# Performance work log

Hardware: AMD Instinct MI355X
Metric: run time of the kernel (lower is better)

## Reference

```python
import jax, jax.numpy as jnp
import numpy as np

HID = 5120       # hidden_size
H = 32           # num_heads (TP shard)
Q_RANK = 1536    # q_lora_rank
KV_RANK = 512    # kv_lora_rank
D_NOPE = 128     # qk_nope_head_dim
D_ROPE = 64      # qk_rope_head_dim
DV = 128         # v_head_dim
Q_HEAD = D_NOPE + D_ROPE
T = 2048
EPS = 1e-6
ROPE_BASE = 10000.0
SCALE = Q_HEAD ** -0.5
NEG = jnp.finfo(jnp.float32).min


def rmsnorm(x, w):
    return x * jax.lax.rsqrt(jnp.mean(x * x, axis=-1, keepdims=True) + EPS) * w


def rope(x, pos):
    # half-split (GPT-NeoX style) rotary; the torch module permutes weights in
    # _update_pe so that interleaved RoPE becomes exactly this half-split form.
    half = x.shape[-1] // 2
    inv = 1.0 / (ROPE_BASE ** (jnp.arange(half, dtype=jnp.float32) / half))
    ang = pos.astype(jnp.float32)[:, None] * inv          # [T, half]
    cos, sin = jnp.cos(ang), jnp.sin(ang)
    if x.ndim == 3:                                       # [T, H, D]
        cos, sin = cos[:, None, :], sin[:, None, :]
    x1, x2 = jnp.split(x, 2, axis=-1)
    return jnp.concatenate([x1 * cos - x2 * sin, x2 * cos + x1 * sin], axis=-1)


def setup_inputs() -> dict:
    key = jax.random.key(0)
    ks = jax.random.split(key, 10)
    s = 0.02
    return {
        'hidden_states': jax.random.normal(ks[0], (1, T, HID), jnp.float32),
        'position_ids': jnp.arange(T, dtype=jnp.int64),
        'w_q_a': jax.random.normal(ks[1], (Q_RANK, HID), jnp.float32) * s,
        'q_a_ln_w': jnp.ones((Q_RANK,), jnp.float32),
        'w_q_b': jax.random.normal(ks[2], (H * Q_HEAD, Q_RANK), jnp.float32) * s,
        'w_kv_a': jax.random.normal(ks[3], (KV_RANK + D_ROPE, HID), jnp.float32) * s,
        'kv_a_ln_w': jnp.ones((KV_RANK,), jnp.float32),
        'w_kc': jax.random.normal(ks[4], (H, D_NOPE, KV_RANK), jnp.float32) * s,
        'w_vc': jax.random.normal(ks[5], (H, KV_RANK, DV), jnp.float32) * s,
        'w_o': jax.random.normal(ks[6], (HID, H * DV), jnp.float32) * s,
    }


def reference(hidden_states, position_ids, w_q_a, q_a_ln_w, w_q_b, w_kv_a,
              kv_a_ln_w, w_kc, w_vc, w_o):
    h = hidden_states[0]                                   # [T, HID]
    t = h.shape[0]
    # q low-rank path: q_a_proj -> rmsnorm -> q_b_proj
    q = rmsnorm(h @ w_q_a.T, q_a_ln_w) @ w_q_b.T           # [T, H*Q_HEAD]
    q = q.reshape(t, H, Q_HEAD)
    q_nope, q_pe = q[..., :D_NOPE], q[..., D_NOPE:]
    # absorb kv_b (w_kc): project q into the latent kv space
    q_lat = jnp.einsum('thn,hnk->thk', q_nope, w_kc)       # [T, H, KV_RANK]
    # kv low-rank path (MQA-style shared latent)
    ckv_full = h @ w_kv_a.T                                # [T, KV_RANK+D_ROPE]
    ckv = rmsnorm(ckv_full[:, :KV_RANK], kv_a_ln_w)        # [T, KV_RANK]
    k_pe = rope(ckv_full[:, KV_RANK:], position_ids)       # [T, D_ROPE]
    q_pe = rope(q_pe, position_ids)                        # [T, H, D_ROPE]
    # full query/key in latent+pe space; key/value shared across heads
    qf = jnp.concatenate([q_lat, q_pe], axis=-1)           # [T, H, KV_RANK+D_ROPE]
    kf = jnp.concatenate([ckv, k_pe], axis=-1)             # [T, KV_RANK+D_ROPE]
    scores = jnp.einsum('thd,sd->hts', qf, kf) * SCALE     # [H, T, T]
    causal = jnp.tril(jnp.ones((t, t), dtype=bool))
    scores = jnp.where(causal[None], scores, NEG)
    p = jax.nn.softmax(scores, axis=-1)
    o = jnp.einsum('hts,sk->thk', p, ckv)                  # [T, H, KV_RANK]
    o = jnp.einsum('thk,hkv->thv', o, w_vc)                # [T, H, DV]
    out = o.reshape(t, H * DV) @ w_o.T                     # [T, HID]
    return out[None]
```

## Files before the change

### kernel.cpp

```cpp
#include <hip/hip_runtime.h>
#include <hip/hip_bf16.h>
#include <type_traits>

typedef __attribute__((ext_vector_type(8))) short short8;
typedef __attribute__((ext_vector_type(4))) float f32x4;
using bf16 = __hip_bfloat16;

#define T_SEQ 2048
#define NH 32
#define SCALE_F 0.07216878364870323f

__device__ inline unsigned short f2bf(float f) {
    unsigned u = __builtin_bit_cast(unsigned, f);
    return (unsigned short)((u + 0x7fffu + ((u >> 16) & 1u)) >> 16);
}

__device__ inline void gload_lds16(const void* g, void* l) {
    __builtin_amdgcn_global_load_lds(
        (const __attribute__((address_space(1))) unsigned*)g,
        (__attribute__((address_space(3))) unsigned*)l, 16, 0, 0);
}

template <typename TC>
__global__ __launch_bounds__(512, 2) void gemm8p_kernel(
    const bf16* __restrict__ A, const bf16* __restrict__ B, TC* __restrict__ C,
    int K, int lda, int ldb, int ldc)
{
    extern __shared__ char Lds[];
    const int nwg = gridDim.x * gridDim.y;
    const int lin = blockIdx.y * gridDim.x + blockIdx.x;
    const int lin2 = (lin & 7) * (nwg >> 3) + (lin >> 3);
    const int bm = (lin2 / gridDim.x) * 256, bn = (lin2 % gridDim.x) * 256;
    const int tid = threadIdx.x, lane = tid & 63, w = tid >> 6;
    const int l15 = lane & 15, lg = lane >> 4;
    const int wmr = (w >> 2) * 64;
    const int wnc = (w & 3) * 32;
    const int lrh = lane >> 3;
    const int scolb = ((lane & 7) * 16) ^ ((lane >> 3) << 4);
    const int rdswz = (l15 & 7) << 4;
    const bf16* Ab = A + (long)bm * lda;
    const bf16* Bb = B + (long)bn * ldb;
    const int nt = K >> 6;

    auto stage_half = [&](int tt, int isB, int h) {
        const int buf = tt & 1;
        const int k0 = (tt >= nt ? tt - nt : tt) << 6;
        const bf16* Base = isB ? Bb : Ab;
        const int ld = isB ? ldb : lda;
        const char* g = (const char*)Base
            + ((long)(h * 128 + w * 8 + lrh) * ld + k0) * 2 + scolb;
        char* l = Lds + buf * 65536 + isB * 32768 + h * 16384 + w * 1024;
        gload_lds16(g, l);
        gload_lds16(g + (long)128 * ld, l + 8192);
    };

    f32x4 acc[4][4][2] = {};
    stage_half(0, 0, 0); stage_half(0, 1, 1); stage_half(0, 0, 1);
    stage_half(0, 1, 0); stage_half(1, 0, 0); stage_half(1, 1, 1);
    asm volatile("s_waitcnt vmcnt(4)" ::: "memory");
    __builtin_amdgcn_s_barrier();

    for (int t = 0; t < nt; ++t) {
        const char* Bufp = Lds + (t & 1) * 65536;
        short8 aF[4][2], bF[2][2];
        #define ARD(mh, fi, ks) \
            (*(const short8*)(Bufp + (mh) * 16384 + (wmr + (fi) * 16 + l15) * 128 \
                              + (((ks) * 64 + lg * 16) ^ rdswz)))
        #define BRD(nh, nj, ks) \
            (*(const short8*)(Bufp + 32768 + (nh) * 16384 + (wnc + (nj) * 16 + l15) * 128 \
                              + (((ks) * 64 + lg * 16) ^ rdswz)))
        #define MFMA16(q) \
            __builtin_amdgcn_s_setprio(1); \
            _Pragma("unroll") for (int ks = 0; ks < 2; ++ks) \
            _Pragma("unroll") for (int fi = 0; fi < 4; ++fi) \
            _Pragma("unroll") for (int nj = 0; nj < 2; ++nj) \
                acc[q][fi][nj] = __builtin_amdgcn_mfma_f32_16x16x32_bf16( \
                    aF[fi][ks], bF[nj][ks], acc[q][fi][nj], 0, 0, 0); \
            __builtin_amdgcn_s_setprio(0);

        #pragma unroll
        for (int fi = 0; fi < 4; ++fi) { aF[fi][0] = ARD(0, fi, 0); aF[fi][1] = ARD(0, fi, 1); }
        #pragma unroll
        for (int nj = 0; nj < 2; ++nj) { bF[nj][0] = BRD(0, nj, 0); bF[nj][1] = BRD(0, nj, 1); }
        stage_half(t + 1, 0, 1);
        asm volatile("s_waitcnt lgkmcnt(8)" ::: "memory");
        __builtin_amdgcn_s_barrier();
        asm volatile("s_waitcnt lgkmcnt(0)" ::: "memory");
        __builtin_amdgcn_sched_barrier(0);
        MFMA16(0)
        __builtin_amdgcn_s_barrier();
        #pragma unroll
        for (int nj = 0; nj < 2; ++nj) { bF[nj][0] = BRD(1, nj, 0); bF[nj][1] = BRD(1, nj, 1); }
        stage_half(t + 1, 1, 0);
        __builtin_amdgcn_s_barrier();
        asm volatile("s_waitcnt lgkmcnt(0)" ::: "memory");
        __builtin_amdgcn_sched_barrier(0);
        MFMA16(1)
        __builtin_amdgcn_s_barrier();
        #pragma unroll
        for (int fi = 0; fi < 4; ++fi) { aF[fi][0] = ARD(1, fi, 0); aF[fi][1] = ARD(1, fi, 1); }
        stage_half(t + 2, 0, 0);
        __builtin_amdgcn_s_barrier();
        asm volatile("s_waitcnt lgkmcnt(0)" ::: "memory");
        __builtin_amdgcn_sched_barrier(0);
        MFMA16(2)
        __builtin_amdgcn_s_barrier();
        #pragma unroll
        for (int nj = 0; nj < 2; ++nj) { bF[nj][0] = BRD(0, nj, 0); bF[nj][1] = BRD(0, nj, 1); }
        stage_half(t + 2, 1, 1);
        __builtin_amdgcn_s_barrier();
        asm volatile("s_waitcnt lgkmcnt(0)" ::: "memory");
        __builtin_amdgcn_sched_barrier(0);
        MFMA16(3)
        asm volatile("s_waitcnt vmcnt(4)" ::: "memory");
        __builtin_amdgcn_s_barrier();
        #undef ARD
        #undef BRD
        #undef MFMA16
    }
    asm volatile("s_waitcnt vmcnt(0)" ::: "memory");
    const int QMH[4] = {0, 0, 1, 1}, QNH[4] = {0, 1, 1, 0};
    #pragma unroll
    for (int q = 0; q < 4; ++q)
        #pragma unroll
        for (int fi = 0; fi < 4; ++fi)
            #pragma unroll
            for (int nj = 0; nj < 2; ++nj)
                #pragma unroll
                for (int i = 0; i < 4; ++i) {
                    const int row = bm + QMH[q] * 128 + wmr + fi * 16 + lg * 4 + i;
                    const int col = bn + QNH[q] * 128 + wnc + nj * 16 + l15;
                    if constexpr (std::is_same<TC, float>::value)
                        C[(long)row * ldc + col] = acc[q][fi][nj][i];
                    else
                        ((unsigned short*)C)[(long)row * ldc + col] = f2bf(acc[q][fi][nj][i]);
                }
}

template <typename TC>
__global__ __launch_bounds__(256, 2) void gemmhw_kernel(
    const bf16* __restrict__ A, const bf16* __restrict__ B, TC* __restrict__ C,
    int K, int lda, int ldb, int ldc,
    long aStride, long bStride, long cStride)
{
    const int z = blockIdx.z;
    A += (long)z * aStride; B += (long)z * bStride; C += (long)z * cStride;
    const int bm = blockIdx.y * 256, bn = blockIdx.x * 128;
    __shared__ __align__(16) short As[2][256 * 32];
    __shared__ __align__(16) short Bs[2][128 * 32];
    const int tid = threadIdx.x, lane = tid & 63, w = tid >> 6;
    const int l15 = lane & 15, lg = lane >> 4;
    const int wm = w >> 1, wn = w & 1;
    const int sx = (lane & 7) ^ (lane >> 3);
    const int lrh = lane >> 3;
    const int srp = sx >> 2;
    const int scol = (sx & 3) * 8;
    const bf16* Ab = A + (long)bm * lda;
    const bf16* Bb = B + (long)bn * ldb;

    auto stage = [&](int buf, int k0) {
        #pragma unroll
        for (int jj = 0; jj < 4; ++jj) {
            const int j = w * 4 + jj;
            const int srow = 2 * (j * 8 + lrh) + srp;
            gload_lds16(Ab + (long)srow * lda + k0 + scol, &As[buf][j * 512]);
        }
        #pragma unroll
        for (int jj = 0; jj < 2; ++jj) {
            const int j = w * 2 + jj;
            const int srow = 2 * (j * 8 + lrh) + srp;
            gload_lds16(Bb + (long)srow * ldb + k0 + scol, &Bs[buf][j * 512]);
        }
    };

    const int rslot = ((((l15 & 1) << 2) | lg) ^ (l15 >> 1)) << 4;
    const int lrow_lo = l15 >> 1;
    f32x4 acc[8][4] = {};
    const int nt = K >> 5;
    stage(0, 0);
    for (int t = 0; t < nt; ++t) {
        if (t + 1 < nt) {
            stage((t + 1) & 1, (t + 1) << 5);
            asm volatile("s_waitcnt vmcnt(6)" ::: "memory");
        } else {
            asm volatile("s_waitcnt vmcnt(0)" ::: "memory");
        }
        __builtin_amdgcn_s_barrier();
        __builtin_amdgcn_sched_barrier(0);
        const char* Ap = (const char*)&As[t & 1][0];
        const char* Bp = (const char*)&Bs[t & 1][0];
        short8 af[8], bf[4];
        #pragma unroll
        for (int fi = 0; fi < 8; ++fi)
            af[fi] = *(const short8*)(Ap + (wm * 64 + fi * 8 + lrow_lo) * 128 + rslot);
        #pragma unroll
        for (int nj = 0; nj < 4; ++nj)
            bf[nj] = *(const short8*)(Bp + (wn * 32 + nj * 8 + lrow_lo) * 128 + rslot);
        #pragma unroll
        for (int fi = 0; fi < 8; ++fi)
            #pragma unroll
            for (int nj = 0; nj < 4; ++nj)
                acc[fi][nj] = __builtin_amdgcn_mfma_f32_16x16x32_bf16(
                    af[fi], bf[nj], acc[fi][nj], 0, 0, 0);
        asm volatile("s_waitcnt lgkmcnt(0)" ::: "memory");
        __builtin_amdgcn_sched_barrier(0);
        __builtin_amdgcn_s_barrier();
        __builtin_amdgcn_sched_barrier(0);
    }
    #pragma unroll
    for (int fi = 0; fi < 8; ++fi)
        #pragma unroll
        for (int nj = 0; nj < 4; ++nj)
            #pragma unroll
            for (int i = 0; i < 4; ++i) {
                const int row = bm + wm * 128 + fi * 16 + lg * 4 + i;
                const int col = bn + wn * 64 + nj * 16 + l15;
                if constexpr (std::is_same<TC, float>::value)
                    C[(long)row * ldc + col] = acc[fi][nj][i];
                else
                    ((unsigned short*)C)[(long)row * ldc + col] = f2bf(acc[fi][nj][i]);
            }
}

template <typename TC>
__global__ __launch_bounds__(512, 4) void gemm8w_kernel(
    const bf16* __restrict__ A, const bf16* __restrict__ B, TC* __restrict__ C,
    int K, int lda, int ldb, int ldc,
    long aStride, long bStride, long cStride)
{
    const int z = blockIdx.z;
    A += (long)z * aStride; B += (long)z * bStride; C += (long)z * cStride;
    const int nwg = gridDim.x * gridDim.y;
    const int lin = blockIdx.y * gridDim.x + blockIdx.x;
    const int lin2 = (lin & 7) * (nwg >> 3) + (lin >> 3);
    const int bm = (lin2 / gridDim.x) * 128, bn = (lin2 % gridDim.x) * 128;
    __shared__ __align__(16) short As[2][128 * 64];
    __shared__ __align__(16) short Bs[2][128 * 64];
    const int tid = threadIdx.x, lane = tid & 63, w = tid >> 6;
    const int l15 = lane & 15, lg = lane >> 4;
    const int wm = w >> 1, wn = w & 1;
    const int c0 = w * 2, c1 = w * 2 + 1;
    const int srow0 = c0 * 8 + (lane >> 3), srow1 = c1 * 8 + (lane >> 3);
    const int scol = ((lane & 7) * 16) ^ ((lane >> 3) << 4);
    const bf16* Ab = A + (long)bm * lda;
    const bf16* Bb = B + (long)bn * ldb;

    auto stage = [&](int buf, int k0) {
        const char* ag = (const char*)(Ab + k0);
        const char* bg = (const char*)(Bb + k0);
        gload_lds16(ag + (long)srow0 * (lda * 2) + scol, &As[buf][c0 * 512]);
        gload_lds16(ag + (long)srow1 * (lda * 2) + scol, &As[buf][c1 * 512]);
        gload_lds16(bg + (long)srow0 * (ldb * 2) + scol, &Bs[buf][c0 * 512]);
        gload_lds16(bg + (long)srow1 * (ldb * 2) + scol, &Bs[buf][c1 * 512]);
    };

    const int swz = (l15 & 7) << 4;
    f32x4 acc[2][4] = {};
    const int nt = K >> 6;
    stage(0, 0);
    for (int t = 0; t < nt; ++t) {
        if (t + 1 < nt) {
            stage((t + 1) & 1, (t + 1) << 6);
            asm volatile("s_waitcnt vmcnt(4)" ::: "memory");
        } else {
            asm volatile("s_waitcnt vmcnt(0)" ::: "memory");
        }
        __builtin_amdgcn_s_barrier();
        __builtin_amdgcn_sched_barrier(0);
        const char* Ap = (const char*)&As[t & 1][0];
        const char* Bp = (const char*)&Bs[t & 1][0];
        short8 af[2][2], bfv[4][2];
        #pragma unroll
        for (int fi = 0; fi < 2; ++fi)
            #pragma unroll
            for (int ks = 0; ks < 2; ++ks)
                af[fi][ks] = *(const short8*)(Ap + (wm * 32 + fi * 16 + l15) * 128
                                              + ((ks * 64 + lg * 16) ^ swz));
        #pragma unroll
        for (int nj = 0; nj < 4; ++nj)
            #pragma unroll
            for (int ks = 0; ks < 2; ++ks)
                bfv[nj][ks] = *(const short8*)(Bp + (wn * 64 + nj * 16 + l15) * 128
                                               + ((ks * 64 + lg * 16) ^ swz));
        #pragma unroll
        for (int ks = 0; ks < 2; ++ks)
            #pragma unroll
            for (int fi = 0; fi < 2; ++fi)
                #pragma unroll
                for (int nj = 0; nj < 4; ++nj)
                    acc[fi][nj] = __builtin_amdgcn_mfma_f32_16x16x32_bf16(
                        af[fi][ks], bfv[nj][ks], acc[fi][nj], 0, 0, 0);
        asm volatile("s_waitcnt lgkmcnt(0)" ::: "memory");
        __builtin_amdgcn_sched_barrier(0);
        __builtin_amdgcn_s_barrier();
        __builtin_amdgcn_sched_barrier(0);
    }
    #pragma unroll
    for (int fi = 0; fi < 2; ++fi)
        #pragma unroll
        for (int nj = 0; nj < 4; ++nj)
            #pragma unroll
            for (int i = 0; i < 4; ++i) {
                const int row = bm + wm * 32 + fi * 16 + lg * 4 + i;
                const int col = bn + wn * 64 + nj * 16 + l15;
                if constexpr (std::is_same<TC, float>::value)
                    C[(long)row * ldc + col] = acc[fi][nj][i];
                else
                    ((unsigned short*)C)[(long)row * ldc + col] = f2bf(acc[fi][nj][i]);
            }
}

__global__ __launch_bounds__(256) void cvt_kernel(
    const float* __restrict__ in, bf16* __restrict__ out, long n, float scale)
{
    const long i = ((long)blockIdx.x * 256 + threadIdx.x) * 8;
    if (i >= n) return;
    f32x4 a = *(const f32x4*)(in + i), b = *(const f32x4*)(in + i + 4);
    short8 r;
    r[0] = (short)f2bf(a[0] * scale); r[1] = (short)f2bf(a[1] * scale);
    r[2] = (short)f2bf(a[2] * scale); r[3] = (short)f2bf(a[3] * scale);
    r[4] = (short)f2bf(b[0] * scale); r[5] = (short)f2bf(b[1] * scale);
    r[6] = (short)f2bf(b[2] * scale); r[7] = (short)f2bf(b[3] * scale);
    *(short8*)(out + i) = r;
}

__global__ __launch_bounds__(256) void tconv_kernel(
    const float* __restrict__ in, bf16* __restrict__ out)
{
    const int h = blockIdx.z, k0 = blockIdx.x * 32, d0 = blockIdx.y * 32;
    __shared__ float t[32][33];
    const int r = threadIdx.x >> 5, c = threadIdx.x & 31;
    const float* ip = in + ((long)h * 512 + k0) * 128 + d0;
    #pragma unroll
    for (int it = 0; it < 4; ++it)
        t[r + 8 * it][c] = ip[(long)(r + 8 * it) * 128 + c];
    __syncthreads();
    bf16* op = out + ((long)h * 128 + d0) * 512 + k0;
    #pragma unroll
    for (int it = 0; it < 4; ++it)
        op[(long)(r + 8 * it) * 512 + c] = __float2bfloat16(t[c][r + 8 * it]);
}

__global__ __launch_bounds__(256) void rmsnorm_kernel(
    bf16* __restrict__ x, const float* __restrict__ w, int C, int ld)
{
    bf16* row = x + (long)blockIdx.x * ld;
    float ss = 0.f;
    for (int i = threadIdx.x; i < C; i += 256) {
        float v = __bfloat162float(row[i]);
        ss += v * v;
    }
    #pragma unroll
    for (int m = 1; m < 64; m <<= 1) ss += __shfl_xor(ss, m, 64);
    __shared__ float red[4];
    if ((threadIdx.x & 63) == 0) red[threadIdx.x >> 6] = ss;
    __syncthreads();
    ss = red[0] + red[1] + red[2] + red[3];
    float scale = rsqrtf(ss / (float)C + 1e-6f);
    for (int i = threadIdx.x; i < C; i += 256) {
        float v = __bfloat162float(row[i]);
        row[i] = __float2bfloat16(v * scale * w[i]);
    }
}

__global__ __launch_bounds__(256) void ropeq_kernel(bf16* __restrict__ q)
{
    const int t = blockIdx.x;
    #pragma unroll
    for (int it = 0; it < 4; ++it) {
        const int pair = threadIdx.x + 256 * it;
        const int h = pair >> 5, i = pair & 31;
        bf16* base = q + ((long)t * NH + h) * 192;
        float x1 = __bfloat162float(base[128 + i]);
        float x2 = __bfloat162float(base[160 + i]);
        float inv = powf(10000.f, -(float)i / 32.f);
        float ang = (float)t * inv, s, c;
        sincosf(ang, &s, &c);
        base[128 + i] = __float2bfloat16(x1 * c - x2 * s);
        base[160 + i] = __float2bfloat16(x2 * c + x1 * s);
    }
}

__global__ __launch_bounds__(1024) void ropek_kernel(
    const bf16* __restrict__ ckv, bf16* __restrict__ kf, int ld)
{
    const int t = blockIdx.x;
    const int h = threadIdx.x >> 5, i = threadIdx.x & 31;
    float x1 = __bfloat162float(ckv[(long)t * ld + 512 + i]);
    float x2 = __bfloat162float(ckv[(long)t * ld + 544 + i]);
    float inv = powf(10000.f, -(float)i / 32.f);
    float ang = (float)t * inv, s, c;
    sincosf(ang, &s, &c);
    bf16* kb = kf + ((long)h * T_SEQ + t) * 192;
    kb[128 + i] = __float2bfloat16(x1 * c - x2 * s);
    kb[160 + i] = __float2bfloat16(x2 * c + x1 * s);
}

__global__ __launch_bounds__(256, 2) void attn_kernel(
    const bf16* __restrict__ Q,
    const bf16* __restrict__ Kf,
    const bf16* __restrict__ Vt,
    bf16* __restrict__ O,
    const float* __restrict__ WOin, bf16* __restrict__ WOout)
{
    if (blockIdx.x >= 512) {
        const long base = ((long)blockIdx.x - 512) * 16384 + threadIdx.x * 8;
        #pragma unroll
        for (int it = 0; it < 8; ++it) {
            const long i = base + (long)it * 2048;
            f32x4 a = *(const f32x4*)(WOin + i), b = *(const f32x4*)(WOin + i + 4);
            short8 r;
            r[0] = (short)f2bf(a[0]); r[1] = (short)f2bf(a[1]);
            r[2] = (short)f2bf(a[2]); r[3] = (short)f2bf(a[3]);
            r[4] = (short)f2bf(b[0]); r[5] = (short)f2bf(b[1]);
            r[6] = (short)f2bf(b[2]); r[7] = (short)f2bf(b[3]);
            *(short8*)(WOout + i) = r;
        }
        return;
    }
    const int lin = blockIdx.x;
    const int h = (lin & 7) + 8 * ((lin >> 3) & 3);
    const int qraw = lin >> 5;
    const int qblk = (qraw < 8) ? (2 * qraw) : (31 - 2 * qraw);
    const int q0 = qblk * 128;
    const int tid = threadIdx.x, lane = tid & 63, w = tid >> 6;
    const int l15 = lane & 15, lg = lane >> 4;
    const int qw = q0 + w * 32;
    __shared__ __align__(16) short Ks[2][64 * 192];
    __shared__ __align__(16) short Vs[2][128 * 64];

    int ksoff[6];
    #pragma unroll
    for (int j = 0; j < 6; ++j) {
        int o = (w * 6 + j) * 1024 + lane * 16;
        int row = o / 384, col = o % 384;
        ksoff[j] = row * 384 + (col ^ ((row & 7) << 4));
    }
    const int vrow8 = lane >> 3;
    const int vscol = ((lane & 7) * 16) ^ (vrow8 << 4);

    short8 qf[2][6];
    #pragma unroll
    for (int qi = 0; qi < 2; ++qi) {
        const bf16* qp = Q + (long)(qw + qi * 16 + l15) * (NH * 192) + (long)h * 192;
        #pragma unroll
        for (int c = 0; c < 6; ++c) qf[qi][c] = *(const short8*)(qp + c * 32 + lg * 8);
    }

    f32x4 oacc[2][8] = {};
    float mst[2] = {-INFINITY, -INFINITY};
    float lst[2] = {0.f, 0.f};

    const char* kbase0 = (const char*)Kf + (long)h * T_SEQ * 384;
    const char* vbase0 = (const char*)Vt + (long)h * 128 * (T_SEQ * 2);
    const int swz = (l15 & 7) << 4;
    const int nt = (q0 + 128) >> 6;

    auto stage = [&](int t) {
        char* KsB = (char*)&Ks[t & 1][0];
        char* VsB = (char*)&Vs[t & 1][0];
        const char* kb = kbase0 + (long)(t * 64) * 384;
        #pragma unroll
        for (int j = 0; j < 6; ++j)
            gload_lds16(kb + ksoff[j], KsB + (w * 6 + j) * 1024);
        const char* vb = vbase0 + (long)(t * 64) * 2 + vscol;
        #pragma unroll
        for (int j = 0; j < 4; ++j) {
            const int c = w * 4 + j;
            gload_lds16(vb + (long)(c * 8 + vrow8) * (T_SEQ * 2), VsB + c * 1024);
        }
    };

    stage(0);
    for (int t = 0; t < nt; ++t) {
        const int s0 = t * 64;
        if (t + 1 < nt) {
            stage(t + 1);
            asm volatile("s_waitcnt vmcnt(10)" ::: "memory");
        } else {
            asm volatile("s_waitcnt vmcnt(0)" ::: "memory");
        }
        __builtin_amdgcn_s_barrier();
        __builtin_amdgcn_sched_barrier(0);
        if (s0 <= qw + 31) {
            const char* KsB = (const char*)&Ks[t & 1][0];
            const char* VsB = (const char*)&Vs[t & 1][0];
            f32x4 st[2][4] = {};
            __builtin_amdgcn_s_setprio(1);
            #pragma unroll
            for (int cb = 0; cb < 4; ++cb) {
                const int krow = cb * 16 + l15;
                #pragma unroll
                for (int c = 0; c < 6; ++c) {
                    short8 kfr = *(const short8*)(KsB + krow * 384
                                                  + ((c * 64 + lg * 16) ^ swz));
                    st[0][cb] = __builtin_amdgcn_mfma_f32_16x16x32_bf16(kfr, qf[0][c], st[0][cb], 0, 0, 0);
                    st[1][cb] = __builtin_amdgcn_mfma_f32_16x16x32_bf16(kfr, qf[1][c], st[1][cb], 0, 0, 0);
                }
            }
            __builtin_amdgcn_s_setprio(0);
            float pmaxv[2];
            #pragma unroll
            for (int qi = 0; qi < 2; ++qi) {
                const int qg = qw + qi * 16 + l15;
                float pmax = -INFINITY;
                #pragma unroll
                for (int cb = 0; cb < 4; ++cb)
                    #pragma unroll
                    for (int i = 0; i < 4; ++i) {
                        const int kv = s0 + cb * 16 + lg * 4 + i;
                        float v = (kv <= qg) ? st[qi][cb][i] : -INFINITY;
                        st[qi][cb][i] = v;
                        pmax = fmaxf(pmax, v);
                    }
                pmax = fmaxf(pmax, __shfl_xor(pmax, 16, 64));
                pmax = fmaxf(pmax, __shfl_xor(pmax, 32, 64));
                pmaxv[qi] = pmax;
            }
            const bool full = !__all((pmaxv[0] - mst[0] <= 8.f) &&
                                     (pmaxv[1] - mst[1] <= 8.f));
            short8 pb[2][2];
            #pragma unroll
            for (int qi = 0; qi < 2; ++qi) {
                float mm;
                if (full) {
                    const float newm = fmaxf(mst[qi], pmaxv[qi]);
                    mm = (newm == -INFINITY) ? 0.f : newm;
                    const float alpha = __expf(mst[qi] - mm);
                    lst[qi] *= alpha;
                    mst[qi] = newm;
                    #pragma unroll
                    for (int mb = 0; mb < 8; ++mb) oacc[qi][mb] *= alpha;
                } else {
                    mm = mst[qi];
                }
                float ps = 0.f;
                #pragma unroll
                for (int cb = 0; cb < 4; ++cb)
                    #pragma unroll
                    for (int i = 0; i < 4; ++i) {
                        const float e = __expf(st[qi][cb][i] - mm);
                        st[qi][cb][i] = e; ps += e;
                    }
                ps += __shfl_xor(ps, 16, 64);
                ps += __shfl_xor(ps, 32, 64);
                lst[qi] += ps;
                #pragma unroll
                for (int hh = 0; hh < 2; ++hh) {
                    unsigned pk[4];
                    #pragma unroll
                    for (int i = 0; i < 4; ++i)
                        pk[i] = (unsigned)f2bf(st[qi][2 * hh][i])
                              | ((unsigned)f2bf(st[qi][2 * hh + 1][i]) << 16);
                    #pragma unroll
                    for (int j = 0; j < 8; ++j) {
                        const int src = l15 + (((2 * lg + (j >> 2)) & 3) << 4);
                        const unsigned u = (unsigned)__shfl((int)pk[j & 3], src, 64);
                        pb[qi][hh][j] = (short)((lg >> 1) ? (u >> 16) : (u & 0xffffu));
                    }
                }
            }
            __builtin_amdgcn_s_setprio(1);
            #pragma unroll
            for (int mb = 0; mb < 8; ++mb) {
                const int vrow = mb * 16 + l15;
                #pragma unroll
                for (int hh = 0; hh < 2; ++hh) {
                    short8 vfr = *(const short8*)(VsB + vrow * 128
                                                  + ((hh * 64 + lg * 16) ^ swz));
                    oacc[0][mb] = __builtin_amdgcn_mfma_f32_16x16x32_bf16(vfr, pb[0][hh], oacc[0][mb], 0, 0, 0);
                    oacc[1][mb] = __builtin_amdgcn_mfma_f32_16x16x32_bf16(vfr, pb[1][hh], oacc[1][mb], 0, 0, 0);
                }
            }
            __builtin_amdgcn_s_setprio(0);
        }
        __builtin_amdgcn_sched_barrier(0);
        __builtin_amdgcn_s_barrier();
    }
    #pragma unroll
    for (int qi = 0; qi < 2; ++qi) {
        const float inv = 1.f / lst[qi];
        const int qg = qw + qi * 16 + l15;
        #pragma unroll
        for (int mb = 0; mb < 8; ++mb)
            #pragma unroll
            for (int i = 0; i < 4; ++i) {
                const int dv = mb * 16 + lg * 4 + i;
                O[(long)qg * (NH * 128) + h * 128 + dv] = __float2bfloat16(oacc[qi][mb][i] * inv);
            }
    }
}

extern "C" void kernel_launch(void* const* d_in, const int* in_sizes, int n_in,
                              void* d_out, int out_size, void* d_ws, size_t ws_size,
                              hipStream_t stream)
{
    const float* hidden    = (const float*)d_in[0];
    const float* w_q_a     = (const float*)d_in[2];
    const float* q_a_ln_w  = (const float*)d_in[3];
    const float* w_q_b     = (const float*)d_in[4];
    const float* w_kv_a    = (const float*)d_in[5];
    const float* kv_a_ln_w = (const float*)d_in[6];
    const float* w_kc      = (const float*)d_in[7];
    const float* w_vc      = (const float*)d_in[8];
    const float* w_o       = (const float*)d_in[9];
    float* out = (float*)d_out;

    bf16* qckv  = (bf16*)d_ws;
    bf16* qbuf  = qckv  + (long)T_SEQ * 2176;
    bf16* kf    = qbuf  + (long)T_SEQ * 6144;
    bf16* vt    = kf    + (long)NH * T_SEQ * 192;
    bf16* ov    = vt    + (long)NH * 128 * T_SEQ;
    bf16* hb    = ov    + (long)T_SEQ * 4096;
    bf16* wqckv = hb    + (long)T_SEQ * 5120;
    bf16* wqb   = wqckv + (long)2176 * 5120;
    bf16* wkc   = wqb   + (long)6144 * 1536;
    bf16* wvct  = wkc   + (long)NH * 128 * 512;
    bf16* wo    = hb;
    bf16* ckv   = qckv + 1536;

    cvt_kernel<<<dim3(5120), 256, 0, stream>>>(hidden, hb, (long)T_SEQ * 5120, 1.f);
    cvt_kernel<<<dim3(3840), 256, 0, stream>>>(w_q_a, wqckv, (long)1536 * 5120, 1.f);
    cvt_kernel<<<dim3(1440), 256, 0, stream>>>(w_kv_a, wqckv + (long)1536 * 5120,
                                               (long)576 * 5120, 1.f);
    hipMemsetAsync(wqckv + (long)2112 * 5120, 0, (long)64 * 5120 * sizeof(bf16), stream);
    cvt_kernel<<<dim3(4608), 256, 0, stream>>>(w_q_b, wqb, (long)6144 * 1536, SCALE_F);
    cvt_kernel<<<dim3(1024), 256, 0, stream>>>(w_kc, wkc, (long)NH * 128 * 512, 1.f);
    tconv_kernel<<<dim3(16, 4, NH), 256, 0, stream>>>(w_vc, wvct);

    gemm8w_kernel<bf16><<<dim3(17, 16, 1), 512, 0, stream>>>(
        hb, wqckv, qckv, 5120, 5120, 5120, 2176, 0, 0, 0);
    rmsnorm_kernel<<<dim3(T_SEQ), 256, 0, stream>>>(qckv, q_a_ln_w, 1536, 2176);
    rmsnorm_kernel<<<dim3(T_SEQ), 256, 0, stream>>>(ckv, kv_a_ln_w, 512, 2176);
    gemm8p_kernel<bf16><<<dim3(24, 8), 512, 131072, stream>>>(
        qckv, wqb, qbuf, 1536, 2176, 1536, 6144);
    ropeq_kernel<<<dim3(T_SEQ), 256, 0, stream>>>(qbuf);
    ropek_kernel<<<dim3(T_SEQ), 1024, 0, stream>>>(ckv, kf, 2176);
    gemmhw_kernel<bf16><<<dim3(1, 8, NH), 256, 0, stream>>>(
        ckv, wkc, kf, 512, 2176, 512, 192,
        0, (long)128 * 512, (long)T_SEQ * 192);
    gemm8p_kernel<bf16><<<dim3(8, 16), 512, 131072, stream>>>(
        wvct, ckv, vt, 512, 512, 2176, 2048);
    attn_kernel<<<dim3(1792), 256, 0, stream>>>(qbuf, kf, vt, ov, w_o, wo);
    gemm8p_kernel<float><<<dim3(20, 8), 512, 131072, stream>>>(
        ov, wo, out, 4096, 4096, 4096, 5120);
}
```

Measured before the change: 447.0 us.

## Fold weight conversions into first GEMM grid and merge two rmsnorm launches

The w_q_b and w_kc fp32-to-bf16 conversions now run on extra workgroups appended to the q/kv-a GEMM grid, so they overlap with the GEMM instead of running as separate launches beforehand. The two rmsnorm launches are merged into one kernel that picks its row set by block index. The XCD-aware tile remapping in both GEMM kernels is removed in favour of plain blockIdx mapping. This cuts launch count, but the extra conversion blocks compete with GEMM blocks for CUs and bandwidth, and dropping the remap may change L2 locality.

Result: no change. 441.7 us (-1.2%).

```diff
diff --git a/kernel.cpp b/kernel.cpp
--- a/kernel.cpp
+++ b/kernel.cpp
@@ -21,16 +21,23 @@
         (__attribute__((address_space(3))) unsigned*)l, 16, 0, 0);
 }
 
+__device__ inline void cvt8(const float* in, bf16* out, long v, float scale) {
+    f32x4 a = *(const f32x4*)(in + v * 8), b = *(const f32x4*)(in + v * 8 + 4);
+    short8 r;
+    r[0] = (short)f2bf(a[0] * scale); r[1] = (short)f2bf(a[1] * scale);
+    r[2] = (short)f2bf(a[2] * scale); r[3] = (short)f2bf(a[3] * scale);
+    r[4] = (short)f2bf(b[0] * scale); r[5] = (short)f2bf(b[1] * scale);
+    r[6] = (short)f2bf(b[2] * scale); r[7] = (short)f2bf(b[3] * scale);
+    *(short8*)(out + v * 8) = r;
+}
+
 template <typename TC>
 __global__ __launch_bounds__(512, 2) void gemm8p_kernel(
     const bf16* __restrict__ A, const bf16* __restrict__ B, TC* __restrict__ C,
     int K, int lda, int ldb, int ldc)
 {
     extern __shared__ char Lds[];
-    const int nwg = gridDim.x * gridDim.y;
-    const int lin = blockIdx.y * gridDim.x + blockIdx.x;
-    const int lin2 = (lin & 7) * (nwg >> 3) + (lin >> 3);
-    const int bm = (lin2 / gridDim.x) * 256, bn = (lin2 % gridDim.x) * 256;
+    const int bm = blockIdx.y * 256, bn = blockIdx.x * 256;
     const int tid = threadIdx.x, lane = tid & 63, w = tid >> 6;
     const int l15 = lane & 15, lg = lane >> 4;
     const int wmr = (w >> 2) * 64;
@@ -222,21 +229,29 @@
             }
 }
 
+#define GW_NXT 17
+#define GW_EXX 8
 template <typename TC>
 __global__ __launch_bounds__(512, 4) void gemm8w_kernel(
     const bf16* __restrict__ A, const bf16* __restrict__ B, TC* __restrict__ C,
     int K, int lda, int ldb, int ldc,
-    long aStride, long bStride, long cStride)
-{
-    const int z = blockIdx.z;
-    A += (long)z * aStride; B += (long)z * bStride; C += (long)z * cStride;
-    const int nwg = gridDim.x * gridDim.y;
-    const int lin = blockIdx.y * gridDim.x + blockIdx.x;
-    const int lin2 = (lin & 7) * (nwg >> 3) + (lin >> 3);
-    const int bm = (lin2 / gridDim.x) * 128, bn = (lin2 % gridDim.x) * 128;
+    const float* __restrict__ cv1in, bf16* __restrict__ cv1out, long n1v, float s1,
+    const float* __restrict__ cv2in, bf16* __restrict__ cv2out, long n2v)
+{
+    const int tid = threadIdx.x;
+    if (blockIdx.x >= GW_NXT) {
+        const int cb = (blockIdx.x - GW_NXT) * gridDim.y + blockIdx.y;
+        const long stride = (long)GW_EXX * gridDim.y * 512;
+        for (long v = (long)cb * 512 + tid; v < n1v + n2v; v += stride) {
+            if (v < n1v) cvt8(cv1in, cv1out, v, s1);
+            else         cvt8(cv2in, cv2out, v - n1v, 1.f);
+        }
+        return;
+    }
+    const int bm = blockIdx.y * 128, bn = blockIdx.x * 128;
     __shared__ __align__(16) short As[2][128 * 64];
     __shared__ __align__(16) short Bs[2][128 * 64];
-    const int tid = threadIdx.x, lane = tid & 63, w = tid >> 6;
+    const int lane = tid & 63, w = tid >> 6;
     const int l15 = lane & 15, lg = lane >> 4;
     const int wm = w >> 1, wn = w & 1;
     const int c0 = w * 2, c1 = w * 2 + 1;
@@ -313,15 +328,9 @@
 __global__ __launch_bounds__(256) void cvt_kernel(
     const float* __restrict__ in, bf16* __restrict__ out, long n, float scale)
 {
-    const long i = ((long)blockIdx.x * 256 + threadIdx.x) * 8;
-    if (i >= n) return;
-    f32x4 a = *(const f32x4*)(in + i), b = *(const f32x4*)(in + i + 4);
-    short8 r;
-    r[0] = (short)f2bf(a[0] * scale); r[1] = (short)f2bf(a[1] * scale);
-    r[2] = (short)f2bf(a[2] * scale); r[3] = (short)f2bf(a[3] * scale);
-    r[4] = (short)f2bf(b[0] * scale); r[5] = (short)f2bf(b[1] * scale);
-    r[6] = (short)f2bf(b[2] * scale); r[7] = (short)f2bf(b[3] * scale);
-    *(short8*)(out + i) = r;
+    const long i = (long)blockIdx.x * 256 + threadIdx.x;
+    if (i * 8 >= n) return;
+    cvt8(in, out, i, scale);
 }
 
 __global__ __launch_bounds__(256) void tconv_kernel(
@@ -341,10 +350,15 @@
         op[(long)(r + 8 * it) * 512 + c] = __float2bfloat16(t[c][r + 8 * it]);
 }
 
-__global__ __launch_bounds__(256) void rmsnorm_kernel(
-    bf16* __restrict__ x, const float* __restrict__ w, int C, int ld)
-{
-    bf16* row = x + (long)blockIdx.x * ld;
+__global__ __launch_bounds__(256) void rmsnorm2_kernel(
+    bf16* __restrict__ x1, const float* __restrict__ w1, int C1,
+    bf16* __restrict__ x2, const float* __restrict__ w2, int C2, int ld)
+{
+    bf16* row;
+    const float* w;
+    int C;
+    if (blockIdx.x < 2048) { row = x1 + (long)blockIdx.x * ld; w = w1; C = C1; }
+    else { row = x2 + (long)(blockIdx.x - 2048) * ld; w = w2; C = C2; }
     float ss = 0.f;
     for (int i = threadIdx.x; i < C; i += 256) {
         float v = __bfloat162float(row[i]);
@@ -404,18 +418,10 @@
     const float* __restrict__ WOin, bf16* __restrict__ WOout)
 {
     if (blockIdx.x >= 512) {
-        const long base = ((long)blockIdx.x - 512) * 16384 + threadIdx.x * 8;
-        #pragma unroll
-        for (int it = 0; it < 8; ++it) {
-            const long i = base + (long)it * 2048;
-            f32x4 a = *(const f32x4*)(WOin + i), b = *(const f32x4*)(WOin + i + 4);
-            short8 r;
-            r[0] = (short)f2bf(a[0]); r[1] = (short)f2bf(a[1]);
-            r[2] = (short)f2bf(a[2]); r[3] = (short)f2bf(a[3]);
-            r[4] = (short)f2bf(b[0]); r[5] = (short)f2bf(b[1]);
-            r[6] = (short)f2bf(b[2]); r[7] = (short)f2bf(b[3]);
-            *(short8*)(WOout + i) = r;
-        }
+        const long base = ((long)blockIdx.x - 512) * 2048 + threadIdx.x;
+        #pragma unroll
+        for (int it = 0; it < 8; ++it)
+            cvt8(WOin, WOout, base + (long)it * 256, 1.f);
         return;
     }
     const int lin = blockIdx.x;
@@ -624,14 +630,14 @@
     cvt_kernel<<<dim3(1440), 256, 0, stream>>>(w_kv_a, wqckv + (long)1536 * 5120,
                                                (long)576 * 5120, 1.f);
     hipMemsetAsync(wqckv + (long)2112 * 5120, 0, (long)64 * 5120 * sizeof(bf16), stream);
-    cvt_kernel<<<dim3(4608), 256, 0, stream>>>(w_q_b, wqb, (long)6144 * 1536, SCALE_F);
-    cvt_kernel<<<dim3(1024), 256, 0, stream>>>(w_kc, wkc, (long)NH * 128 * 512, 1.f);
     tconv_kernel<<<dim3(16, 4, NH), 256, 0, stream>>>(w_vc, wvct);
 
-    gemm8w_kernel<bf16><<<dim3(17, 16, 1), 512, 0, stream>>>(
-        hb, wqckv, qckv, 5120, 5120, 5120, 2176, 0, 0, 0);
-    rmsnorm_kernel<<<dim3(T_SEQ), 256, 0, stream>>>(qckv, q_a_ln_w, 1536, 2176);
-    rmsnorm_kernel<<<dim3(T_SEQ), 256, 0, stream>>>(ckv, kv_a_ln_w, 512, 2176);
+    gemm8w_kernel<bf16><<<dim3(GW_NXT + GW_EXX, 16, 1), 512, 0, stream>>>(
+        hb, wqckv, qckv, 5120, 5120, 5120, 2176,
+        w_q_b, wqb, (long)6144 * 1536 / 8, SCALE_F,
+        w_kc, wkc, (long)NH * 128 * 512 / 8);
+    rmsnorm2_kernel<<<dim3(4096), 256, 0, stream>>>(
+        qckv, q_a_ln_w, 1536, ckv, kv_a_ln_w, 512, 2176);
     gemm8p_kernel<bf16><<<dim3(24, 8), 512, 131072, stream>>>(
         qckv, wqb, qbuf, 1536, 2176, 1536, 6144);
     ropeq_kernel<<<dim3(T_SEQ), 256, 0, stream>>>(qbuf);
```
